# Kernel optimization log

Hardware: AMD Instinct MI355X
Metric: run time of the kernel (lower is better)

## Reference

```python
import jax, jax.numpy as jnp
import numpy as np
from jax import lax

B, N = 16, 4096
S1, S2, K = 512, 256, 32
EPS = 1e-5


def setup_inputs() -> dict:
    key = jax.random.key(0)
    ks = jax.random.split(key, 8)
    p = lambda k, shape: jax.random.normal(k, shape, jnp.float32) * 0.05
    return {
        "x": jax.random.normal(ks[0], (B, 3, N), jnp.float32),
        "w1": p(ks[1], (64, 3)),
        "w2": p(ks[2], (64, 64)),
        "g1": jnp.ones(64, jnp.float32), "b1": jnp.zeros(64, jnp.float32),
        "g2": jnp.ones(64, jnp.float32), "b2": jnp.zeros(64, jnp.float32),
        "sg1_w1": p(ks[3], (128, 128)), "sg1_w2": p(ks[4], (128, 128)),
        "sg1_g1": jnp.ones(128, jnp.float32), "sg1_b1": jnp.zeros(128, jnp.float32),
        "sg1_g2": jnp.ones(128, jnp.float32), "sg1_b2": jnp.zeros(128, jnp.float32),
        "sg2_w1": p(ks[5], (256, 256)), "sg2_w2": p(ks[6], (256, 256)),
        "sg2_g1": jnp.ones(256, jnp.float32), "sg2_b1": jnp.zeros(256, jnp.float32),
        "sg2_g2": jnp.ones(256, jnp.float32), "sg2_b2": jnp.zeros(256, jnp.float32),
    }


def fps(coords, s):
    # furthest point sampling, starts at index 0 (as pointnet2 CUDA kernel)
    Bc, Nc, _ = coords.shape
    def step(carry, _):
        dist, far = carry
        centroid = jnp.take_along_axis(coords, far[:, None, None], axis=1)  # [B,1,3]
        d = jnp.sum((coords - centroid) ** 2, -1)                            # [B,N]
        dist = jnp.minimum(dist, d)
        return (dist, jnp.argmax(dist, -1)), far
    init = (jnp.full((Bc, Nc), 1e10, coords.dtype), jnp.zeros((Bc,), jnp.int32))
    _, idxs = lax.scan(step, init, None, length=s)
    return idxs.T  # [B,s]


def gather(pts, idx):
    # pts [B,N,C], idx [B,...] -> [B,...,C]
    return jax.vmap(lambda p, i: p[i])(pts, idx)


def sqdist(a, b):
    # [B,S,3],[B,N,3] -> [B,S,N]
    return (jnp.sum(a ** 2, -1)[..., None] + jnp.sum(b ** 2, -1)[:, None, :]
            - 2.0 * jnp.einsum('bsc,bnc->bsn', a, b))


def bn_relu_grouped(y, g, b):
    # y [B,s,k,O]; BatchNorm1d over (B*s, O, k) => stats over (0,1,2)
    m = y.mean((0, 1, 2), keepdims=True)
    v = y.var((0, 1, 2), keepdims=True)
    return jax.nn.relu((y - m) / jnp.sqrt(v + EPS) * g + b)


def sg_block(f_bnc, coords, s, w1, g1, b1, w2, g2, b2):
    # f_bnc [B,N,C]; coords [B,N,3]
    fidx = fps(coords, s)                      # [B,s]
    new_xyz = gather(coords, fidx)             # [B,s,3]
    new_feat = gather(f_bnc, fidx)             # [B,s,C]
    d = sqdist(new_xyz, coords)                # [B,s,N]
    _, knn_idx = lax.top_k(-d, K)              # [B,s,K]
    grouped = gather(f_bnc, knn_idx)           # [B,s,K,C]
    center = new_feat[:, :, None]              # [B,s,1,C]
    agg = jnp.concatenate([grouped - center,
                           jnp.broadcast_to(center, grouped.shape)], -1)  # [B,s,K,2C]
    y = bn_relu_grouped(jnp.einsum('bskd,od->bsko', agg, w1), g1, b1)
    y = bn_relu_grouped(jnp.einsum('bskd,od->bsko', y, w2), g2, b2)
    return new_xyz, y.max(2)                   # [B,s,O]


def point_cbr(f, w, g, b):
    # f [B,C,N]; conv1d k=1 + BN (stats over (0,2)) + relu
    y = jnp.einsum('bcn,oc->bon', f, w)
    m = y.mean((0, 2), keepdims=True)
    v = y.var((0, 2), keepdims=True)
    return jax.nn.relu((y - m) / jnp.sqrt(v + EPS) * g[None, :, None] + b[None, :, None])


def reference(x, w1, w2, g1, b1, g2, b2,
              sg1_w1, sg1_w2, sg1_g1, sg1_b1, sg1_g2, sg1_b2,
              sg2_w1, sg2_w2, sg2_g1, sg2_b1, sg2_g2, sg2_b2):
    xyz = x.transpose(0, 2, 1)                                  # [B,N,3]
    f = point_cbr(point_cbr(x, w1, g1, b1), w2, g2, b2)         # [B,64,N]
    xyz1, f1 = sg_block(f.transpose(0, 2, 1), xyz, S1,
                        sg1_w1, sg1_g1, sg1_b1, sg1_w2, sg1_g2, sg1_b2)  # f1 [B,S1,128]
    _, f2 = sg_block(f1, xyz1, S2,
                     sg2_w1, sg2_g1, sg2_b1, sg2_w2, sg2_g2, sg2_b2)     # [B,S2,256]
    return f2.transpose(0, 2, 1)                                # [B,256,S2]
```

## Files before the change

kernel.cpp:

```cpp
#include <hip/hip_runtime.h>

#define EPSF 1e-5f
#define NBINS 64
#define STATS_REGION 32768

using short8  = __attribute__((ext_vector_type(8))) short;
using float4v = __attribute__((ext_vector_type(4))) float;

__device__ __forceinline__ unsigned short f2bf(float f){
    unsigned u = __float_as_uint(f);
    unsigned r = u + 0x7FFFu + ((u >> 16) & 1u);
    return (unsigned short)(r >> 16);
}
__device__ __forceinline__ float bf2f(unsigned short h){
    return __uint_as_float(((unsigned)h) << 16);
}
__device__ __forceinline__ unsigned monou(float f){
    unsigned u = __float_as_uint(f);
    return u ^ (((unsigned)((int)u >> 31)) | 0x80000000u);
}

template<int CTRL, int RMASK>
__device__ __forceinline__ float fmax_dpp(float x){
    int xi = __float_as_int(x);
    int yi = __builtin_amdgcn_update_dpp(xi, xi, CTRL, RMASK, 0xf, false);
    return fmaxf(x, __int_as_float(yi));
}
__device__ __forceinline__ float wave_max_dpp(float x){
    x = fmax_dpp<0x111, 0xf>(x);
    x = fmax_dpp<0x112, 0xf>(x);
    x = fmax_dpp<0x114, 0xf>(x);
    x = fmax_dpp<0x118, 0xf>(x);
    x = fmax_dpp<0x142, 0xa>(x);
    x = fmax_dpp<0x143, 0xc>(x);
    return __int_as_float(__builtin_amdgcn_readlane(__float_as_int(x), 63));
}

__device__ __forceinline__ void compute_ss(const float* __restrict__ st,
                                           const float* __restrict__ g,
                                           const float* __restrict__ bb,
                                           float* lss, int C, float invCnt,
                                           int t, int TPB){
    for (int c = t; c < C; c += TPB){
        float s = 0.f, q = 0.f;
        for (int bin = 0; bin < NBINS; bin++){
            s += st[bin * 2 * C + c];
            q += st[bin * 2 * C + C + c];
        }
        float m = s * invCnt;
        float v = q * invCnt - m * m;
        float sc = g[c] / sqrtf(v + EPSF);
        lss[c] = sc;
        lss[C + c] = bb[c] - m * sc;
    }
}

template<int NP, int SO, int AW, bool STRIDED>
__device__ void fps_body(char* smem, const float* __restrict__ coords,
                         int* __restrict__ fidx, float* __restrict__ xyz_out, int b){
    float* lx = (float*)smem;
    float* ly = lx + NP;
    float* lz = ly + NP;
    unsigned long long* red = (unsigned long long*)(lz + NP);
    const int t = threadIdx.x;
    const float* cb = coords + (size_t)b * 3 * NP;
    constexpr int PS = NP / 256;
    #pragma unroll
    for (int i = 0; i < PS; i++){
        int n = i * 256 + t;
        float X, Y, Z;
        if (STRIDED){ X = cb[n]; Y = cb[NP + n]; Z = cb[2*NP + n]; }
        else        { X = cb[n*3]; Y = cb[n*3+1]; Z = cb[n*3+2]; }
        lx[n] = X; ly[n] = Y; lz[n] = Z;
    }
    __syncthreads();
    if (AW == 1 && t >= 64) return;
    constexpr int TPB = AW * 64;
    constexpr int P = NP / TPB;
    float px[P], py[P], pz[P], dist[P];
    #pragma unroll
    for (int i = 0; i < P; i++){
        int n = t * P + i;
        px[i] = lx[n]; py[i] = ly[n]; pz[i] = lz[n];
        dist[i] = 1e10f;
    }
    int cur = 0;
    for (int it = 0; it < SO; ++it){
        if (t == 0){
            fidx[b * SO + it] = cur;
            float* xo = xyz_out + ((size_t)b * SO + it) * 3;
            xo[0] = lx[cur]; xo[1] = ly[cur]; xo[2] = lz[cur];
        }
        float cx = lx[cur], cy = ly[cur], cz = lz[cur];
        float bd = -1.f;
        int bn = 0;
        {
            #pragma clang fp contract(off)
            #pragma unroll
            for (int i = 0; i < P; i++){
                float dx = px[i] - cx, dy = py[i] - cy, dz = pz[i] - cz;
                float d = (dx*dx + dy*dy) + dz*dz;
                float nd = fminf(dist[i], d);
                dist[i] = nd;
                if (nd > bd){ bd = nd; bn = t * P + i; }
            }
        }
        float wm = wave_max_dpp(bd);
        unsigned long long msk = __ballot(bd == wm);
        int wl = (int)(__ffsll(msk) - 1);
        int n_w = __builtin_amdgcn_readlane(bn, wl);
        if constexpr (AW == 1){
            cur = n_w;
        } else {
            int par = it & 1;
            if ((t & 63) == 0){
                red[par * AW + (t >> 6)] = ((unsigned long long)__float_as_uint(wm) << 32)
                                         | (unsigned)(0xFFFFFFFFu - (unsigned)n_w);
            }
            __syncthreads();
            unsigned long long best = red[par * AW];
            #pragma unroll
            for (int j = 1; j < AW; j++){
                unsigned long long v = red[par * AW + j];
                best = best > v ? best : v;
            }
            cur = (int)(0xFFFFFFFFu - (unsigned)(best & 0xFFFFFFFFull));
        }
    }
}

template<int NC, int SO, bool STRIDED>
__device__ void knn_body(const float* __restrict__ coords,
                         const float* __restrict__ samp,
                         int* __restrict__ knno, int row){
    const int b = row / SO, s = row % SO;
    const int lane = threadIdx.x & 63;
    const float* cb = coords + (size_t)b * 3 * NC;
    const float* a = samp + ((size_t)b * SO + s) * 3;
    float ax = a[0], ay = a[1], az = a[2];
    float asq = ax*ax + ay*ay + az*az;
    constexpr int J = NC / 64;
    unsigned long long t8[8];
    #pragma unroll
    for (int i = 0; i < 8; i++) t8[i] = ~0ULL;
    for (int j = 0; j < J; j++){
        int n = j * 64 + lane;
        float bx, by, bz;
        if (STRIDED){ bx = cb[n]; by = cb[NC + n]; bz = cb[2*NC + n]; }
        else        { bx = cb[n*3]; by = cb[n*3+1]; bz = cb[n*3+2]; }
        float bsq = bx*bx + by*by + bz*bz;
        float dot = ax*bx + ay*by + az*bz;
        float d = (asq + bsq) - 2.0f * dot;
        unsigned long long key = ((unsigned long long)monou(d) << 32) | (unsigned)n;
        if (key < t8[7]){
            t8[7] = key;
            #pragma unroll
            for (int i = 6; i >= 0; i--){
                if (t8[i] > t8[i+1]){ unsigned long long tm = t8[i]; t8[i] = t8[i+1]; t8[i+1] = tm; }
            }
        }
    }
    unsigned long long cur = t8[0];
    int myout = 0;
    bool bad = false;
    int popped = 0;
    for (int r = 0; r < 32; r++){
        unsigned long long m = cur;
        #pragma unroll
        for (int o2 = 32; o2 > 0; o2 >>= 1){
            unsigned long long v = __shfl_xor(m, o2, 64);
            m = m < v ? m : v;
        }
        if (lane == r) myout = (int)(unsigned)(m & 0xFFFFFFFFull);
        if (cur == m){
            #pragma unroll
            for (int i = 0; i < 7; i++) t8[i] = t8[i+1];
            t8[7] = ~0ULL;
            cur = t8[0];
            popped++;
            if (J > 8 && popped == 8 && r < 31) bad = true;
        }
    }
    if (__any(bad)){
        unsigned long long last = 0;
        for (int r = 0; r < 32; r++){
            unsigned long long mk = ~0ULL;
            for (int j = 0; j < J; j++){
                int n = j * 64 + lane;
                float bx, by, bz;
                if (STRIDED){ bx = cb[n]; by = cb[NC + n]; bz = cb[2*NC + n]; }
                else        { bx = cb[n*3]; by = cb[n*3+1]; bz = cb[n*3+2]; }
                float bsq = bx*bx + by*by + bz*bz;
                float dot = ax*bx + ay*by + az*bz;
                float d = (asq + bsq) - 2.0f * dot;
                unsigned long long key = ((unsigned long long)monou(d) << 32) | (unsigned)n;
                if (key > last && key < mk) mk = key;
            }
            unsigned long long m = mk;
            #pragma unroll
            for (int o2 = 32; o2 > 0; o2 >>= 1){
                unsigned long long v = __shfl_xor(m, o2, 64);
                m = m < v ? m : v;
            }
            if (lane == r) myout = (int)(unsigned)(m & 0xFFFFFFFFull);
            last = m;
        }
    }
    if (lane < 32) knno[((size_t)b * SO + s) * 32 + lane] = myout;
}

__device__ void pc_body(char* smem, const float* __restrict__ x,
                        const float* __restrict__ w1, const float* __restrict__ w2,
                        const float* __restrict__ g1, const float* __restrict__ b1,
                        const float* __restrict__ xmom, float* __restrict__ y2t, int blk){
    float* w1s  = (float*)smem;
    float* wt   = w1s + 192;
    float* lss1 = wt + 4096;
    float* hS   = lss1 + 128;
    int t = threadIdx.x;
    if (t < 192) w1s[t] = w1[t];
    for (int i = t; i < 4096; i += 256){ int o = i & 63, c = i >> 6; wt[c*64+o] = w2[o*64+c]; }
    __syncthreads();
    if (t < 64){
        float mu0 = xmom[0] * (1.f/65536.f), mu1 = xmom[1] * (1.f/65536.f), mu2 = xmom[2] * (1.f/65536.f);
        float M00 = xmom[3] * (1.f/65536.f), M01 = xmom[4] * (1.f/65536.f), M02 = xmom[5] * (1.f/65536.f);
        float M11 = xmom[6] * (1.f/65536.f), M12 = xmom[7] * (1.f/65536.f), M22 = xmom[8] * (1.f/65536.f);
        float a = w1s[t*3], b = w1s[t*3+1], c = w1s[t*3+2];
        float mo = a*mu0 + b*mu1 + c*mu2;
        float e2 = a*a*M00 + b*b*M11 + c*c*M22 + 2.f*(a*b*M01 + a*c*M02 + b*c*M12);
        float var = e2 - mo*mo;
        float sc = g1[t] / sqrtf(var + EPSF);
        lss1[t] = sc;
        lss1[64 + t] = b1[t] - mo * sc;
    }
    __syncthreads();
    int p = t & 63, cg = t >> 6;
    int point = blk * 64 + p;
    int b = point >> 12, n = point & 4095;
    const float* xb = x + (size_t)b * 12288;
    float x0 = xb[n], x1 = xb[4096 + n], x2 = xb[8192 + n];
    #pragma unroll
    for (int i = 0; i < 16; i++){
        int c = cg * 16 + i;
        float y1 = x0 * w1s[c*3] + x1 * w1s[c*3+1] + x2 * w1s[c*3+2];
        hS[p * 65 + c] = fmaxf(y1 * lss1[c] + lss1[64 + c], 0.f);
    }
    __syncthreads();
    float4v acc[4];
    #pragma unroll
    for (int i = 0; i < 4; i++) acc[i] = (float4v){0.f,0.f,0.f,0.f};
    for (int c = 0; c < 64; c++){
        float hv = hS[p * 65 + c];
        #pragma unroll
        for (int i = 0; i < 4; i++){
            float4v w4 = *(const float4v*)&wt[c*64 + cg*16 + i*4];
            acc[i] += hv * w4;
        }
    }
    float* dst = y2t + (size_t)point * 64 + cg * 16;
    #pragma unroll
    for (int i = 0; i < 4; i++) *(float4v*)(dst + i*4) = acc[i];
}


template<int O, int D>
__device__ __forceinline__ void pack_body(const float* __restrict__ w,
                                          unsigned short* __restrict__ pk, int tid){
    constexpr int CH = D / 32;
    constexpr int TOT = (O/16) * CH * 64;
    if (tid >= TOT) return;
    int lane = tid & 63;
    int fc = tid >> 6;
    int ch = fc % CH;
    int ot = fc / CH;
    int o  = ot * 16 + (lane & 15);
    int kb = ch * 32 + (lane >> 4) * 8;
    #pragma unroll
    for (int j = 0; j < 8; j++) pk[(size_t)tid * 8 + j] = f2bf(w[(size_t)o * D + kb + j]);
}

template<int D, int O>
__device__ __forceinline__ void mfma_store_y(const short* A, const short* wp,
                                             unsigned short* Y, float* lsum, float* lsq,
                                             int blk, int t){
    constexpr int RS = D + 8;
    constexpr int CH = D / 32;
    constexpr int OPW = (O / 16) / 4;
    int lane = t & 63, wv = t >> 6;
    int col = lane & 15, quad = lane >> 4;
    for (int oi = 0; oi < OPW; ++oi){
        int ot = wv * OPW + oi;
        for (int mt = 0; mt < 4; ++mt){
            float4v acc = {0.f, 0.f, 0.f, 0.f};
            #pragma unroll
            for (int ch = 0; ch < CH; ++ch){
                short8 a  = *(const short8*)(A + (mt*16 + col) * RS + ch*32 + quad*8);
                short8 bf = *(const short8*)(wp + ((size_t)(ot*CH + ch) * 64 + lane) * 8);
                acc = __builtin_amdgcn_mfma_f32_16x16x32_bf16(a, bf, acc, 0, 0, 0);
            }
            float s4 = 0.f, q4 = 0.f;
            size_t rowbase = (size_t)blk * 64 + mt * 16 + quad * 4;
            #pragma unroll
            for (int r = 0; r < 4; r++){
                float v = acc[r];
                s4 += v; q4 += v * v;
                Y[(rowbase + r) * O + ot * 16 + col] = f2bf(v);
            }
            s4 += __shfl_xor(s4, 16, 64); s4 += __shfl_xor(s4, 32, 64);
            q4 += __shfl_xor(q4, 16, 64); q4 += __shfl_xor(q4, 32, 64);
            if (quad == 0){ lsum[ot*16 + col] += s4; lsq[ot*16 + col] += q4; }
        }
    }
}

template<int D, int O>
__device__ __forceinline__ void mfma_maxmin(const short* A, const short* wp,
                                            float2* mxmn, float* lsum, float* lsq,
                                            int blk, int t){
    constexpr int RS = D + 8;
    constexpr int CH = D / 32;
    constexpr int OPW = (O / 16) / 4;
    int lane = t & 63, wv = t >> 6;
    int col = lane & 15, quad = lane >> 4;
    for (int oi = 0; oi < OPW; ++oi){
        int ot = wv * OPW + oi;
        float mx[2] = {-1e30f, -1e30f}, mn[2] = {1e30f, 1e30f};
        for (int mt = 0; mt < 4; ++mt){
            float4v acc = {0.f, 0.f, 0.f, 0.f};
            #pragma unroll
            for (int ch = 0; ch < CH; ++ch){
                short8 a  = *(const short8*)(A + (mt*16 + col) * RS + ch*32 + quad*8);
                short8 bf = *(const short8*)(wp + ((size_t)(ot*CH + ch) * 64 + lane) * 8);
                acc = __builtin_amdgcn_mfma_f32_16x16x32_bf16(a, bf, acc, 0, 0, 0);
            }
            int g = mt >> 1;
            float s4 = 0.f, q4 = 0.f;
            #pragma unroll
            for (int r = 0; r < 4; r++){
                float v = acc[r];
                s4 += v; q4 += v * v;
                mx[g] = fmaxf(mx[g], v);
                mn[g] = fminf(mn[g], v);
            }
            s4 += __shfl_xor(s4, 16, 64); s4 += __shfl_xor(s4, 32, 64);
            q4 += __shfl_xor(q4, 16, 64); q4 += __shfl_xor(q4, 32, 64);
            if (quad == 0){ lsum[ot*16 + col] += s4; lsq[ot*16 + col] += q4; }
        }
        #pragma unroll
        for (int g = 0; g < 2; g++){
            mx[g] = fmaxf(mx[g], __shfl_xor(mx[g], 16, 64));
            mx[g] = fmaxf(mx[g], __shfl_xor(mx[g], 32, 64));
            mn[g] = fminf(mn[g], __shfl_xor(mn[g], 16, 64));
            mn[g] = fminf(mn[g], __shfl_xor(mn[g], 32, 64));
            if (quad == 0){
                mxmn[((size_t)(blk * 2 + g)) * O + ot * 16 + col] = make_float2(mx[g], mn[g]);
            }
        }
    }
}

template<int DH, int O, int S, int NPTS, int MODE>
__device__ void gemm1_body(char* smem, const void* __restrict__ fsrc,
                           const float* __restrict__ fst, const float* __restrict__ fg,
                           const float* __restrict__ fb, float finv,
                           const int* __restrict__ fidx, const int* __restrict__ knn,
                           const short* __restrict__ wp, unsigned short* __restrict__ Y,
                           float* __restrict__ sums, int blk){
    constexpr int D = 2 * DH;
    constexpr int RS = D + 8;
    short* A    = (short*)smem;
    float* lsum = (float*)(smem + 64*RS*2);
    float* lsq  = lsum + O;
    float* lssf = lsq + O;
    int t = threadIdx.x;
    for (int i = t; i < O; i += 256){ lsum[i] = 0.f; lsq[i] = 0.f; }
    compute_ss(fst, fg, fb, lssf, DH, finv, t, 256);
    __syncthreads();
    for (int g = 0; g < 2; ++g){
        int gid = blk * 2 + g;
        int b = gid / S;
        int cidx = fidx[gid];
        int kk = t >> 3;
        int p  = t & 7;
        int nb = knn[(size_t)gid * 32 + kk];
        constexpr int E = D / 8;
        int d0 = p * E;
        short* row = A + (g * 32 + kk) * RS;
        if (MODE == 1){
            const float* fcp = (const float*)fsrc + ((size_t)b * NPTS + cidx) * DH;
            const float* fnp = (const float*)fsrc + ((size_t)b * NPTS + nb) * DH;
            #pragma unroll
            for (int e = 0; e < E; e++){
                int d = d0 + e;
                float v;
                if (d < DH){
                    float a = fmaxf(fnp[d] * lssf[d] + lssf[DH + d], 0.f);
                    float c = fmaxf(fcp[d] * lssf[d] + lssf[DH + d], 0.f);
                    v = a - c;
                } else {
                    v = fmaxf(fcp[d - DH] * lssf[d - DH] + lssf[DH + d - DH], 0.f);
                }
                row[d] = (short)f2bf(v);
            }
        } else {
            const float2* fcp = (const float2*)fsrc + ((size_t)b * NPTS + cidx) * DH;
            const float2* fnp = (const float2*)fsrc + ((size_t)b * NPTS + nb) * DH;
            #pragma unroll
            for (int e = 0; e < E; e++){
                int d = d0 + e;
                float v;
                if (d < DH){
                    float sc = lssf[d], sh = lssf[DH + d];
                    float2 a2 = fnp[d], c2 = fcp[d];
                    float av = fmaxf((sc > 0.f ? a2.x : a2.y) * sc + sh, 0.f);
                    float cv = fmaxf((sc > 0.f ? c2.x : c2.y) * sc + sh, 0.f);
                    v = av - cv;
                } else {
                    int dd = d - DH;
                    float sc = lssf[dd], sh = lssf[DH + dd];
                    float2 c2 = fcp[dd];
                    v = fmaxf((sc > 0.f ? c2.x : c2.y) * sc + sh, 0.f);
                }
                row[d] = (short)f2bf(v);
            }
        }
    }
    __syncthreads();
    mfma_store_y<D, O>(A, wp, Y, lsum, lsq, blk, t);
    __syncthreads();
    float* dst = sums + (size_t)(blk & (NBINS - 1)) * 2 * O;
    for (int i = t; i < O; i += 256){
        atomicAdd(&dst[i], lsum[i]);
        atomicAdd(&dst[O + i], lsq[i]);
    }
}

template<int D, int O>
__device__ void gemm2m_body(char* smem, const unsigned short* __restrict__ Yin,
                            const float* __restrict__ st, const float* __restrict__ g,
                            const float* __restrict__ bb, float inv,
                            const short* __restrict__ wp, float2* __restrict__ mxmn,
                            float* __restrict__ sums, int blk){
    constexpr int RS = D + 8;
    short* A    = (short*)smem;
    float* lsum = (float*)(smem + 64*RS*2);
    float* lsq  = lsum + O;
    float* lss  = lsq + O;
    int t = threadIdx.x;
    for (int i = t; i < O; i += 256){ lsum[i] = 0.f; lsq[i] = 0.f; }
    compute_ss(st, g, bb, lss, D, inv, t, 256);
    __syncthreads();
    {
        int row = t >> 2;
        int d0 = (t & 3) * (D / 4);
        const unsigned short* src = Yin + ((size_t)blk * 64 + row) * D + d0;
        short* dst = A + row * RS + d0;
        #pragma unroll
        for (int e = 0; e < D/4; e++){
            float v = bf2f(src[e]);
            int d = d0 + e;
            v = fmaxf(v * lss[d] + lss[D + d], 0.f);
            dst[e] = (short)f2bf(v);
        }
    }
    __syncthreads();
    mfma_maxmin<D, O>(A, wp, mxmn, lsum, lsq, blk, t);
    __syncthreads();
    float* dst = sums + (size_t)(blk & (NBINS - 1)) * 2 * O;
    for (int i = t; i < O; i += 256){
        atomicAdd(&dst[i], lsum[i]);
        atomicAdd(&dst[O + i], lsq[i]);
    }
}


__global__ __launch_bounds__(256) void k1_statsx_pack(const float* __restrict__ x,
                                                      float* __restrict__ xmom,
                                                      const float* w1, const float* w2,
                                                      const float* w3, const float* w4,
                                                      unsigned short* p1, unsigned short* p2,
                                                      unsigned short* p3, unsigned short* p4){
    int blk = blockIdx.x, t = threadIdx.x;
    if (blk == 0){
        float a[9] = {0,0,0,0,0,0,0,0,0};
        for (int gid = t; gid < 65536; gid += 256){
            int b = gid >> 12, n = gid & 4095;
            const float* xb = x + (size_t)b * 12288;
            float x0 = xb[n], x1 = xb[4096 + n], x2 = xb[8192 + n];
            a[0] += x0; a[1] += x1; a[2] += x2;
            a[3] += x0*x0; a[4] += x0*x1; a[5] += x0*x2;
            a[6] += x1*x1; a[7] += x1*x2; a[8] += x2*x2;
        }
        __shared__ float red[4][9];
        #pragma unroll
        for (int k = 0; k < 9; k++){
            float v = a[k];
            for (int o = 32; o > 0; o >>= 1) v += __shfl_down(v, o, 64);
            a[k] = v;
        }
        if ((t & 63) == 0){
            #pragma unroll
            for (int k = 0; k < 9; k++) red[t >> 6][k] = a[k];
        }
        __syncthreads();
        if (t == 0){
            #pragma unroll
            for (int k = 0; k < 9; k++)
                xmom[k] = red[0][k] + red[1][k] + red[2][k] + red[3][k];
        }
    } else {
        int pb = blk - 1;
        if (pb < 8)       pack_body<128,128>(w1, p1, pb * 256 + t);
        else if (pb < 16) pack_body<128,128>(w2, p2, (pb - 8) * 256 + t);
        else if (pb < 48) pack_body<256,256>(w3, p3, (pb - 16) * 256 + t);
        else              pack_body<256,256>(w4, p4, (pb - 48) * 256 + t);
    }
}

__global__ __launch_bounds__(256) void k2_fps1_pc(const float* __restrict__ x,
                                                  int* __restrict__ fidx1, float* __restrict__ xyz1,
                                                  const float* w1, const float* w2,
                                                  const float* g1, const float* b1,
                                                  const float* __restrict__ xmom,
                                                  float* __restrict__ y2t){
    extern __shared__ char smem[];
    if (blockIdx.x < 16) fps_body<4096,512,4,true>(smem, x, fidx1, xyz1, blockIdx.x);
    else                 pc_body(smem, x, w1, w2, g1, b1, xmom, y2t, blockIdx.x - 16);
}

__global__ __launch_bounds__(256) void k3_statsy2_knn1(const float* __restrict__ y2t,
                                                       float* __restrict__ stY2,
                                                       const float* __restrict__ x,
                                                       const float* __restrict__ xyz1,
                                                       int* __restrict__ knn1){
    int t = threadIdx.x;
    if (blockIdx.x < 256){
        int blk = blockIdx.x;
        int o = t & 63, rg = t >> 6;
        float s = 0.f, q = 0.f;
        for (int j = 0; j < 64; j++){
            int row = blk * 256 + j * 4 + rg;
            float v = y2t[(size_t)row * 64 + o];
            s += v; q += v * v;
        }
        __shared__ float rs[4][64], rq[4][64];
        rs[rg][o] = s; rq[rg][o] = q;
        __syncthreads();
        if (t < 64){
            float ss = rs[0][t] + rs[1][t] + rs[2][t] + rs[3][t];
            float qq = rq[0][t] + rq[1][t] + rq[2][t] + rq[3][t];
            float* dst = stY2 + (size_t)(blk & (NBINS - 1)) * 128;
            atomicAdd(&dst[t], ss);
            atomicAdd(&dst[64 + t], qq);
        }
    } else {
        int row = (blockIdx.x - 256) * 4 + (t >> 6);
        knn_body<4096,512,true>(x, xyz1, knn1, row);
    }
}

__global__ __launch_bounds__(256) void k4_fps2_gemm1a(const float* __restrict__ xyz1,
                                                      int* __restrict__ fidx2, float* __restrict__ xyz2,
                                                      const float* __restrict__ y2t,
                                                      const float* __restrict__ stY2,
                                                      const float* g2, const float* b2,
                                                      const int* __restrict__ fidx1,
                                                      const int* __restrict__ knn1,
                                                      const short* __restrict__ wp1,
                                                      unsigned short* __restrict__ Y1,
                                                      float* __restrict__ stG1a){
    extern __shared__ char smem[];
    if (blockIdx.x < 16)
        fps_body<512,256,1,false>(smem, xyz1, fidx2, xyz2, blockIdx.x);
    else
        gemm1_body<64,128,512,4096,1>(smem, y2t, stY2, g2, b2, 1.f/65536.f,
                                      fidx1, knn1, wp1, Y1, stG1a, blockIdx.x - 16);
}

__global__ __launch_bounds__(256) void k5_knn2_gemm2ma(const float* __restrict__ xyz1,
                                                       const float* __restrict__ xyz2,
                                                       int* __restrict__ knn2,
                                                       const unsigned short* __restrict__ Y1,
                                                       const float* __restrict__ stG1a,
                                                       const float* s1g1, const float* s1b1,
                                                       const short* __restrict__ wp2,
                                                       float2* __restrict__ mxmn1,
                                                       float* __restrict__ stG2a){
    extern __shared__ char smem[];
    if (blockIdx.x < 1024){
        int row = blockIdx.x * 4 + (threadIdx.x >> 6);
        knn_body<512,256,false>(xyz1, xyz2, knn2, row);
    } else {
        gemm2m_body<128,128>(smem, Y1, stG1a, s1g1, s1b1, 1.f/262144.f,
                             wp2, mxmn1, stG2a, blockIdx.x - 1024);
    }
}

template<int DH, int O, int S, int NPTS, int MODE>
__global__ __launch_bounds__(256) void gemm1_kernel(const void* fsrc, const float* fst,
                                                    const float* fg, const float* fb, float finv,
                                                    const int* fidx, const int* knn,
                                                    const short* wp, unsigned short* Y,
                                                    float* sums){
    extern __shared__ char smem[];
    gemm1_body<DH,O,S,NPTS,MODE>(smem, fsrc, fst, fg, fb, finv, fidx, knn, wp, Y, sums, blockIdx.x);
}

template<int D, int O>
__global__ __launch_bounds__(256) void gemm2m_kernel(const unsigned short* Yin, const float* st,
                                                     const float* g, const float* bb, float inv,
                                                     const short* wp, float2* mxmn, float* sums){
    extern __shared__ char smem[];
    gemm2m_body<D,O>(smem, Yin, st, g, bb, inv, wp, mxmn, sums, blockIdx.x);
}

__global__ __launch_bounds__(256) void final_out_kernel(const float2* __restrict__ mxmn,
                                                        const float* __restrict__ st,
                                                        const float* __restrict__ g,
                                                        const float* __restrict__ bb,
                                                        float inv,
                                                        float* __restrict__ out){
    __shared__ float lss[512];
    __shared__ float tile[64][65];
    int t = threadIdx.x;
    compute_ss(st, g, bb, lss, 256, inv, t, 256);
    __syncthreads();
    int blk = blockIdx.x;
    int b = blk >> 4;
    int ot = (blk >> 2) & 3, stt = blk & 3;
    int o_in = t & 63, sg = t >> 6;
    int o = ot * 64 + o_in;
    float sc = lss[o], sh = lss[256 + o];
    for (int si = 0; si < 16; si++){
        int s = stt * 64 + sg * 16 + si;
        int row = b * 256 + s;
        float2 v2 = mxmn[(size_t)row * 256 + o];
        float v = (sc > 0.f ? v2.x : v2.y) * sc + sh;
        tile[sg * 16 + si][o_in] = fmaxf(v, 0.f);
    }
    __syncthreads();
    int s_in = t & 63, og = t >> 6;
    for (int oj = 0; oj < 16; oj++){
        int oo = ot * 64 + og * 16 + oj;
        out[(size_t)b * 65536 + (size_t)oo * 256 + stt * 64 + s_in] = tile[s_in][og * 16 + oj];
    }
}

extern "C" void kernel_launch(void* const* d_in, const int* in_sizes, int n_in,
                              void* d_out, int out_size, void* d_ws, size_t ws_size,
                              hipStream_t stream) {
    const float* x    = (const float*)d_in[0];
    const float* w1   = (const float*)d_in[1];
    const float* w2   = (const float*)d_in[2];
    const float* g1   = (const float*)d_in[3];
    const float* b1   = (const float*)d_in[4];
    const float* g2   = (const float*)d_in[5];
    const float* b2   = (const float*)d_in[6];
    const float* s1w1 = (const float*)d_in[7];
    const float* s1w2 = (const float*)d_in[8];
    const float* s1g1 = (const float*)d_in[9];
    const float* s1b1 = (const float*)d_in[10];
    const float* s1g2 = (const float*)d_in[11];
    const float* s1b2 = (const float*)d_in[12];
    const float* s2w1 = (const float*)d_in[13];
    const float* s2w2 = (const float*)d_in[14];
    const float* s2g1 = (const float*)d_in[15];
    const float* s2b1 = (const float*)d_in[16];
    const float* s2g2 = (const float*)d_in[17];
    const float* s2b2 = (const float*)d_in[18];
    float* out = (float*)d_out;

    char* ws = (char*)d_ws;
    size_t off = 0;
    auto take = [&](size_t bytes){ size_t r = off; off += (bytes + 255) & ~(size_t)255; return r; };
    float* y2t     = (float*)(ws + take(16u*4096u*64u*4u));
    float2* mxmn1  = (float2*)(ws + take(8192u*128u*8u));
    float2* mxmn2  = (float2*)(ws + take(4096u*256u*8u));
    int*   fidx1   = (int*)  (ws + take(16u*512u*4u));
    float* xyz1    = (float*)(ws + take(16u*512u*3u*4u));
    int*   fidx2   = (int*)  (ws + take(16u*256u*4u));
    float* xyz2    = (float*)(ws + take(16u*256u*3u*4u));
    int*   knn1    = (int*)  (ws + take(16u*512u*32u*4u));
    int*   knn2    = (int*)  (ws + take(16u*256u*32u*4u));
    unsigned short* wp1 = (unsigned short*)(ws + take(128u*128u*2u));
    unsigned short* wp2 = (unsigned short*)(ws + take(128u*128u*2u));
    unsigned short* wp3 = (unsigned short*)(ws + take(256u*256u*2u));
    unsigned short* wp4 = (unsigned short*)(ws + take(256u*256u*2u));
    float* stats   = (float*)(ws + take(6u*STATS_REGION*4u));
    char*  regA    = ws + take(67108864u);
    (void)in_sizes; (void)n_in; (void)out_size; (void)ws_size;

    float* xmom    = stats + 0*STATS_REGION;
    float* stY2    = stats + 1*STATS_REGION;
    float* stG1a   = stats + 2*STATS_REGION;
    float* stG2a   = stats + 3*STATS_REGION;
    float* stG1b   = stats + 4*STATS_REGION;
    float* stG2b   = stats + 5*STATS_REGION;

    unsigned short* Y1 = (unsigned short*)regA;

    hipMemsetAsync(stats, 0, 6u*STATS_REGION*4u, stream);

    k1_statsx_pack<<<81, 256, 0, stream>>>(x, xmom, s1w1, s1w2, s2w1, s2w2, wp1, wp2, wp3, wp4);
    k2_fps1_pc<<<1040, 256, 49216, stream>>>(x, fidx1, xyz1, w1, w2, g1, b1, xmom, y2t);
    k3_statsy2_knn1<<<2304, 256, 0, stream>>>(y2t, stY2, x, xyz1, knn1);
    k4_fps2_gemm1a<<<4112, 256, 18944, stream>>>(xyz1, fidx2, xyz2, y2t, stY2, g2, b2,
                                                 fidx1, knn1, (const short*)wp1, Y1, stG1a);
    k5_knn2_gemm2ma<<<5120, 256, 19456, stream>>>(xyz1, xyz2, knn2, Y1, stG1a, s1g1, s1b1,
                                                  (const short*)wp2, mxmn1, stG2a);
    gemm1_kernel<128,256,256,512,2><<<2048, 256, 36864, stream>>>(
        mxmn1, stG2a, s1g2, s1b2, 1.f/262144.f, fidx2, knn2, (const short*)wp3, Y1, stG1b);
    gemm2m_kernel<256,256><<<2048, 256, 37888, stream>>>(
        Y1, stG1b, s2g1, s2b1, 1.f/131072.f, (const short*)wp4, mxmn2, stG2b);
    final_out_kernel<<<256, 256, 0, stream>>>(mxmn2, stG2b, s2g2, s2b2, 1.f/131072.f, out);
}
```

Before: 979.1 us.

## Fuse y2 BatchNorm statistics into pointwise conv epilogue and shrink stat bins

```diff
diff --git a/kernel.cpp b/kernel.cpp
--- a/kernel.cpp
+++ b/kernel.cpp
@@ -1,8 +1,8 @@
 #include <hip/hip_runtime.h>
 
 #define EPSF 1e-5f
-#define NBINS 64
-#define STATS_REGION 32768
+#define NBINS 16
+#define STATS_REGION 8192
 
 using short8  = __attribute__((ext_vector_type(8))) short;
 using float4v = __attribute__((ext_vector_type(4))) float;
@@ -43,6 +43,7 @@
                                            int t, int TPB){
     for (int c = t; c < C; c += TPB){
         float s = 0.f, q = 0.f;
+        #pragma unroll 4
         for (int bin = 0; bin < NBINS; bin++){
             s += st[bin * 2 * C + c];
             q += st[bin * 2 * C + C + c];
@@ -212,7 +213,8 @@
 __device__ void pc_body(char* smem, const float* __restrict__ x,
                         const float* __restrict__ w1, const float* __restrict__ w2,
                         const float* __restrict__ g1, const float* __restrict__ b1,
-                        const float* __restrict__ xmom, float* __restrict__ y2t, int blk){
+                        const float* __restrict__ xmom, float* __restrict__ y2t,
+                        float* __restrict__ stY2, int blk){
     float* w1s  = (float*)smem;
     float* wt   = w1s + 192;
     float* lss1 = wt + 4096;
@@ -260,6 +262,28 @@
     float* dst = y2t + (size_t)point * 64 + cg * 16;
     #pragma unroll
     for (int i = 0; i < 4; i++) *(float4v*)(dst + i*4) = acc[i];
+    float s16[16], q16[16];
+    #pragma unroll
+    for (int i = 0; i < 16; i++){
+        float v = acc[i >> 2][i & 3];
+        s16[i] = v; q16[i] = v * v;
+    }
+    #pragma unroll
+    for (int i = 0; i < 16; i++){
+        #pragma unroll
+        for (int o = 32; o > 0; o >>= 1){
+            s16[i] += __shfl_xor(s16[i], o, 64);
+            q16[i] += __shfl_xor(q16[i], o, 64);
+        }
+    }
+    if (p == 0){
+        float* sdst = stY2 + (size_t)(blk & (NBINS - 1)) * 128;
+        #pragma unroll
+        for (int i = 0; i < 16; i++){
+            atomicAdd(&sdst[cg * 16 + i], s16[i]);
+            atomicAdd(&sdst[64 + cg * 16 + i], q16[i]);
+        }
+    }
 }
 
 
@@ -522,41 +546,18 @@
                                                   const float* w1, const float* w2,
                                                   const float* g1, const float* b1,
                                                   const float* __restrict__ xmom,
-                                                  float* __restrict__ y2t){
+                                                  float* __restrict__ y2t,
+                                                  float* __restrict__ stY2){
     extern __shared__ char smem[];
     if (blockIdx.x < 16) fps_body<4096,512,4,true>(smem, x, fidx1, xyz1, blockIdx.x);
-    else                 pc_body(smem, x, w1, w2, g1, b1, xmom, y2t, blockIdx.x - 16);
-}
-
-__global__ __launch_bounds__(256) void k3_statsy2_knn1(const float* __restrict__ y2t,
-                                                       float* __restrict__ stY2,
-                                                       const float* __restrict__ x,
-                                                       const float* __restrict__ xyz1,
-                                                       int* __restrict__ knn1){
-    int t = threadIdx.x;
-    if (blockIdx.x < 256){
-        int blk = blockIdx.x;
-        int o = t & 63, rg = t >> 6;
-        float s = 0.f, q = 0.f;
-        for (int j = 0; j < 64; j++){
-            int row = blk * 256 + j * 4 + rg;
-            float v = y2t[(size_t)row * 64 + o];
-            s += v; q += v * v;
-        }
-        __shared__ float rs[4][64], rq[4][64];
-        rs[rg][o] = s; rq[rg][o] = q;
-        __syncthreads();
-        if (t < 64){
-            float ss = rs[0][t] + rs[1][t] + rs[2][t] + rs[3][t];
-            float qq = rq[0][t] + rq[1][t] + rq[2][t] + rq[3][t];
-            float* dst = stY2 + (size_t)(blk & (NBINS - 1)) * 128;
-            atomicAdd(&dst[t], ss);
-            atomicAdd(&dst[64 + t], qq);
-        }
-    } else {
-        int row = (blockIdx.x - 256) * 4 + (t >> 6);
-        knn_body<4096,512,true>(x, xyz1, knn1, row);
-    }
+    else                 pc_body(smem, x, w1, w2, g1, b1, xmom, y2t, stY2, blockIdx.x - 16);
+}
+
+__global__ __launch_bounds__(256) void k3_knn1(const float* __restrict__ x,
+                                               const float* __restrict__ xyz1,
+                                               int* __restrict__ knn1){
+    int row = blockIdx.x * 4 + (threadIdx.x >> 6);
+    knn_body<4096,512,true>(x, xyz1, knn1, row);
 }
 
 __global__ __launch_bounds__(256) void k4_fps2_gemm1a(const float* __restrict__ xyz1,
@@ -702,8 +703,8 @@
     hipMemsetAsync(stats, 0, 6u*STATS_REGION*4u, stream);
 
     k1_statsx_pack<<<81, 256, 0, stream>>>(x, xmom, s1w1, s1w2, s2w1, s2w2, wp1, wp2, wp3, wp4);
-    k2_fps1_pc<<<1040, 256, 49216, stream>>>(x, fidx1, xyz1, w1, w2, g1, b1, xmom, y2t);
-    k3_statsy2_knn1<<<2304, 256, 0, stream>>>(y2t, stY2, x, xyz1, knn1);
+    k2_fps1_pc<<<1040, 256, 49216, stream>>>(x, fidx1, xyz1, w1, w2, g1, b1, xmom, y2t, stY2);
+    k3_knn1<<<2048, 256, 0, stream>>>(x, xyz1, knn1);
     k4_fps2_gemm1a<<<4112, 256, 18944, stream>>>(xyz1, fidx2, xyz2, y2t, stY2, g2, b2,
                                                  fidx1, knn1, (const short*)wp1, Y1, stG1a);
     k5_knn2_gemm2ma<<<5120, 256, 19456, stream>>>(xyz1, xyz2, knn2, Y1, stG1a, s1g1, s1b1,
```

After: 939.9 us. 1.04x faster.
